# Performance work log

Hardware: AMD Instinct MI355X
Metric: run time of the kernel (lower is better)

The kernel has to match this reference:

```python
import jax, jax.numpy as jnp
import numpy as np

DIM, NCOND, K, NFLOWS, HID = 8, 16, 5, 2, 8
TB = 3.0                      # tail bound B
CMAX = NCOND + DIM - 1        # 23, max conditioning width (zero-padded)
MINW = MINH = MIND = 1e-3


def _fcnn(x, W1, b1, W2, b2, W3, b3):
    h = jnp.tanh(x @ W1.T + b1)
    h = jnp.tanh(h @ W2.T + b2)
    return h @ W3.T + b3


def _rqs_fwd(x, uw, uh, ud, tb):
    # x: [N]; uw, uh: [N, K] (already softmaxed+scaled by caller, re-softmaxed
    # here to match the original RQS implementation); ud: [N, K+1] (padded)
    nb = uw.shape[-1]
    widths = MINW + (1.0 - MINW * nb) * jax.nn.softmax(uw, axis=-1)
    cumw = jnp.pad(jnp.cumsum(widths, axis=-1), ((0, 0), (1, 0)))
    cumw = (2.0 * tb) * cumw - tb
    cumw = cumw.at[:, 0].set(-tb).at[:, -1].set(tb)
    widths = cumw[:, 1:] - cumw[:, :-1]
    heights = MINH + (1.0 - MINH * nb) * jax.nn.softmax(uh, axis=-1)
    cumh = jnp.pad(jnp.cumsum(heights, axis=-1), ((0, 0), (1, 0)))
    cumh = (2.0 * tb) * cumh - tb
    cumh = cumh.at[:, 0].set(-tb).at[:, -1].set(tb)
    heights = cumh[:, 1:] - cumh[:, :-1]
    derivs = MIND + jax.nn.softplus(ud)
    # searchsorted with eps on last edge
    idx = (jnp.sum(x[:, None] >= cumw.at[:, -1].add(1e-6), axis=-1) - 1)[:, None]
    take = lambda a: jnp.take_along_axis(a, idx, axis=-1)[:, 0]
    icw, ibw, ich, ih = take(cumw), take(widths), take(cumh), take(heights)
    idelta = take(heights / widths)
    d0, d1 = take(derivs), take(derivs[:, 1:])
    th = (x - icw) / ibw
    t2, tomt = th * th, th * (1.0 - th)
    den = idelta + (d0 + d1 - 2.0 * idelta) * tomt
    z = ich + ih * (idelta * t2 + d0 * tomt) / den
    ld = jnp.log(idelta ** 2 * (d1 * t2 + 2.0 * idelta * tomt + d0 * (1.0 - th) ** 2)) - 2.0 * jnp.log(den)
    return z, ld


def _unconstrained_rqs(x, W, H, D, tb):
    inside = (x >= -tb) & (x <= tb)
    const = float(np.log(np.exp(1.0 - MIND) - 1.0))
    Dp = jnp.pad(D, ((0, 0), (1, 1)), constant_values=const)
    z_in, ld_in = _rqs_fwd(jnp.clip(x, -tb, tb), W, H, Dp, tb)
    return jnp.where(inside, z_in, x), jnp.where(inside, ld_in, 0.0)


def setup_inputs() -> dict:
    key = jax.random.key(0)
    ks = jax.random.split(key, 16)
    N = 524288
    s = 0.3
    inp = {
        "x_inp": jax.random.normal(ks[0], (N, DIM), jnp.float32),
        "cond_inp": jax.random.normal(ks[1], (N, NCOND), jnp.float32),
        # init (base-dist) nets, one per dim; first layer zero-padded to CMAX
        "Wi1": s * jax.random.normal(ks[2], (DIM, HID, CMAX), jnp.float32),
        "bi1": s * jax.random.normal(ks[3], (DIM, HID), jnp.float32),
        "Wi2": s * jax.random.normal(ks[4], (DIM, HID, HID), jnp.float32),
        "bi2": s * jax.random.normal(ks[5], (DIM, HID), jnp.float32),
        "Wi3": s * jax.random.normal(ks[6], (DIM, 2, HID), jnp.float32),
        "bi3": s * jax.random.normal(ks[7], (DIM, 2), jnp.float32),
        # flow nets, per (dim, flow)
        "Wf1": s * jax.random.normal(ks[8], (DIM, NFLOWS, HID, CMAX), jnp.float32),
        "bf1": s * jax.random.normal(ks[9], (DIM, NFLOWS, HID), jnp.float32),
        "Wf2": s * jax.random.normal(ks[10], (DIM, NFLOWS, HID, HID), jnp.float32),
        "bf2": s * jax.random.normal(ks[11], (DIM, NFLOWS, HID), jnp.float32),
        "Wf3": s * jax.random.normal(ks[12], (DIM, NFLOWS, 3 * K - 1, HID), jnp.float32),
        "bf3": s * jax.random.normal(ks[13], (DIM, NFLOWS, 3 * K - 1), jnp.float32),
    }
    return inp


def reference(x_inp, cond_inp, Wi1, bi1, Wi2, bi2, Wi3, bi3,
              Wf1, bf1, Wf2, bf2, Wf3, bf3):
    N = x_inp.shape[0]
    logp_cols = []
    for jd in range(DIM):
        pad = jnp.zeros((N, CMAX - NCOND - jd), x_inp.dtype)
        cond_jd = jnp.concatenate([cond_inp, x_inp[:, :jd], pad], axis=1)  # [N, CMAX]
        # gumbel base-dist params
        outg = _fcnn(cond_jd, Wi1[jd], bi1[jd], Wi2[jd], bi2[jd], Wi3[jd], bi3[jd])
        mu, sig = outg[:, 0], jnp.exp(outg[:, 1])
        x = x_inp[:, jd]
        ld_sum = jnp.zeros((N,), x_inp.dtype)
        for jf in range(NFLOWS):
            out = _fcnn(cond_jd, Wf1[jd, jf], bf1[jd, jf], Wf2[jd, jf], bf2[jd, jf],
                        Wf3[jd, jf], bf3[jd, jf])  # [N, 3K-1]
            W = 2.0 * TB * jax.nn.softmax(out[:, :K], axis=1)
            H = 2.0 * TB * jax.nn.softmax(out[:, K:2 * K], axis=1)
            D = jax.nn.softplus(out[:, 2 * K:])
            x, ld = _unconstrained_rqs(x, W, H, D, TB)
            ld_sum = ld_sum + ld
        z = (x - mu) / sig
        lp = -(z + jnp.exp(-z)) - jnp.log(sig)  # Gumbel log_prob
        lp = jnp.where(jnp.isnan(lp) | jnp.isinf(lp), -100.0, lp)
        logp_cols.append(ld_sum + lp)
    return jnp.sum(jnp.stack(logp_cols, axis=1), axis=1)
```

## Files before the change

### kernel.cpp

```cpp
#include <hip/hip_runtime.h>
#include <math.h>

__device__ __forceinline__ float rcp_(float x) { return __fdividef(1.0f, x); }

__device__ __forceinline__ float tanh_(float x) {
    float t = x * x;
    float p = t + 378.0f;
    p = fmaf(p, t, 17325.0f);
    p = fmaf(p, t, 135135.0f);
    float q = fmaf(28.0f, t, 3150.0f);
    q = fmaf(q, t, 62370.0f);
    q = fmaf(q, t, 135135.0f);
    float r = (x * p) * rcp_(q);
    return fminf(fmaxf(r, -1.0f), 1.0f);
}

__device__ __forceinline__ float sp2_(float x) {
    return __logf(2.0f + __expf(x));
}

__device__ __forceinline__ void dsm5_(float o0, float o1, float o2, float o3, float o4,
                                      float* __restrict__ w) {
    float e0 = __expf(o0), e1 = __expf(o1), e2 = __expf(o2),
          e3 = __expf(o3), e4 = __expf(o4);
    float inv = 6.0f * rcp_(((e0 + e1) + (e2 + e3)) + e4);
    float f0 = __expf(e0 * inv);
    float f1 = __expf(e1 * inv);
    float f2 = __expf(e2 * inv);
    float f3 = __expf(e3 * inv);
    float f4 = __expf(e4 * inv);
    float t = 0.995f * rcp_(((f0 + f1) + (f2 + f3)) + f4);
    w[0] = fmaf(f0, t, 0.001f);
    w[1] = fmaf(f1, t, 0.001f);
    w[2] = fmaf(f2, t, 0.001f);
    w[3] = fmaf(f3, t, 0.001f);
    w[4] = fmaf(f4, t, 0.001f);
}

__global__ __launch_bounds__(512, 4)
void nsf_kernel(const float* __restrict__ x_inp, const float* __restrict__ cond_inp,
                const float* __restrict__ Wi1, const float* __restrict__ bi1,
                const float* __restrict__ Wi2, const float* __restrict__ bi2,
                const float* __restrict__ Wi3, const float* __restrict__ bi3,
                const float* __restrict__ Wf1, const float* __restrict__ bf1,
                const float* __restrict__ Wf2, const float* __restrict__ bf2,
                const float* __restrict__ Wf3, const float* __restrict__ bf3,
                float* __restrict__ out, int N)
{
    const int lane = threadIdx.x;
    const int jd   = threadIdx.y;
    const int jdu  = __builtin_amdgcn_readfirstlane(jd);
    int s = blockIdx.x * 64 + lane;
    int sl = (s < N) ? s : (N - 1);

    float cond[23];
    float xcur;
    {
        const float4* cp = (const float4*)(cond_inp + (size_t)sl * 16);
        float4 c0 = cp[0], c1 = cp[1], c2 = cp[2], c3 = cp[3];
        cond[0]=c0.x;  cond[1]=c0.y;  cond[2]=c0.z;  cond[3]=c0.w;
        cond[4]=c1.x;  cond[5]=c1.y;  cond[6]=c1.z;  cond[7]=c1.w;
        cond[8]=c2.x;  cond[9]=c2.y;  cond[10]=c2.z; cond[11]=c2.w;
        cond[12]=c3.x; cond[13]=c3.y; cond[14]=c3.z; cond[15]=c3.w;

        const float4* xp = (const float4*)(x_inp + (size_t)sl * 8);
        float4 a = xp[0], b = xp[1];
        float xv[8] = {a.x, a.y, a.z, a.w, b.x, b.y, b.z, b.w};
#pragma unroll
        for (int t = 0; t < 7; ++t)
            cond[16 + t] = (t < jd) ? xv[t] : 0.0f;
        xcur = xv[jd];
    }

    float g0, g1;
    {
        const float* W1 = Wi1 + (size_t)jdu * 184;
        const float* b1 = bi1 + jdu * 8;
        const float* W2 = Wi2 + (size_t)jdu * 64;
        const float* b2 = bi2 + jdu * 8;
        const float* W3 = Wi3 + (size_t)jdu * 16;
        const float* b3 = bi3 + jdu * 2;
        float h1[8], h2[8];
#pragma unroll
        for (int i = 0; i < 8; ++i) {
            float a = b1[i];
#pragma unroll
            for (int c = 0; c < 23; ++c) a = fmaf(W1[i * 23 + c], cond[c], a);
            h1[i] = tanh_(a);
        }
#pragma unroll
        for (int i = 0; i < 8; ++i) {
            float a = b2[i];
#pragma unroll
            for (int c = 0; c < 8; ++c) a = fmaf(W2[i * 8 + c], h1[c], a);
            h2[i] = tanh_(a);
        }
        g0 = b3[0]; g1 = b3[1];
#pragma unroll
        for (int c = 0; c < 8; ++c) {
            g0 = fmaf(W3[c], h2[c], g0);
            g1 = fmaf(W3[8 + c], h2[c], g1);
        }
    }

    float ldsum = 0.0f;
#pragma unroll
    for (int jf = 0; jf < 2; ++jf) {
        const int nf = jdu * 2 + jf;
        const float* F1  = Wf1 + (size_t)nf * 184;
        const float* fb1 = bf1 + nf * 8;
        const float* F2  = Wf2 + (size_t)nf * 64;
        const float* fb2 = bf2 + nf * 8;
        const float* F3  = Wf3 + (size_t)nf * 112;
        const float* fb3 = bf3 + nf * 14;

        float h1[8], h2[8];
#pragma unroll
        for (int i = 0; i < 8; ++i) {
            float a = fb1[i];
#pragma unroll
            for (int c = 0; c < 23; ++c) a = fmaf(F1[i * 23 + c], cond[c], a);
            h1[i] = tanh_(a);
        }
#pragma unroll
        for (int i = 0; i < 8; ++i) {
            float a = fb2[i];
#pragma unroll
            for (int c = 0; c < 8; ++c) a = fmaf(F2[i * 8 + c], h1[c], a);
            h2[i] = tanh_(a);
        }
        float o[14];
#pragma unroll
        for (int i = 0; i < 14; ++i) {
            float a = fb3[i];
#pragma unroll
            for (int c = 0; c < 8; ++c) a = fmaf(F3[i * 8 + c], h2[c], a);
            o[i] = a;
        }

        float wv[5], hv[5];
        dsm5_(o[0], o[1], o[2], o[3], o[4], wv);
        dsm5_(o[5], o[6], o[7], o[8], o[9], hv);
        float di1 = sp2_(o[10]) + 0.001f;
        float di2 = sp2_(o[11]) + 0.001f;
        float di3 = sp2_(o[12]) + 0.001f;
        float di4 = sp2_(o[13]) + 0.001f;

        float xc = fminf(fmaxf(xcur, -3.0f), 3.0f);

        float runw = wv[0], runh = hv[0];
        float cwL = -3.0f, chL = -3.0f;
        float cwR = fmaf(6.0f, runw, -3.0f);
        float chR = fmaf(6.0f, runh, -3.0f);
        float icw = cwL, ibw = cwR - cwL, ich = chL, ihh = chR - chL;
        float d0 = 1.0f, d1 = di1;
#pragma unroll
        for (int k = 1; k < 5; ++k) {
            cwL = cwR; chL = chR;
            runw += wv[k]; runh += hv[k];
            cwR = (k == 4) ? 3.0f : fmaf(6.0f, runw, -3.0f);
            chR = (k == 4) ? 3.0f : fmaf(6.0f, runh, -3.0f);
            float dk0 = (k == 1) ? di1 : (k == 2) ? di2 : (k == 3) ? di3 : di4;
            float dk1 = (k == 1) ? di2 : (k == 2) ? di3 : (k == 3) ? di4 : 1.0f;
            bool sel = (xc >= cwL);
            icw = sel ? cwL : icw;
            ibw = sel ? (cwR - cwL) : ibw;
            ich = sel ? chL : ich;
            ihh = sel ? (chR - chL) : ihh;
            d0  = sel ? dk0 : d0;
            d1  = sel ? dk1 : d1;
        }

        float rb     = rcp_(ibw);
        float idelta = ihh * rb;
        float th     = (xc - icw) * rb;
        float t2     = th * th;
        float omt    = 1.0f - th;
        float tomt   = th * omt;
        float den    = fmaf(fmaf(-2.0f, idelta, d0 + d1), tomt, idelta);
        float rden   = rcp_(den);
        float xn     = fmaf(ihh * fmaf(idelta, t2, d0 * tomt), rden, ich);
        float num    = (idelta * idelta) *
                       fmaf(d1, t2, fmaf(idelta + idelta, tomt, d0 * (omt * omt)));
        float ldi    = __logf((num * rden) * rden);

        bool inside = (xcur >= -3.0f) && (xcur <= 3.0f);
        xcur  = inside ? xn : xcur;
        ldsum = inside ? (ldsum + ldi) : ldsum;
    }

    float z  = (xcur - g0) * __expf(-g1);
    float ez = __expf(-z);
    float lp = -(z + ez) - g1;
    if (isnan(lp) || isinf(lp)) lp = -100.0f;
    float col = ldsum + lp;

    __shared__ float red[8][64];
    red[jd][lane] = col;
    __syncthreads();
    if (jd == 0 && s < N) {
        float acc = red[0][lane];
#pragma unroll
        for (int j = 1; j < 8; ++j) acc += red[j][lane];
        out[s] = acc;
    }
}

extern "C" void kernel_launch(void* const* d_in, const int* in_sizes, int n_in,
                              void* d_out, int out_size, void* d_ws, size_t ws_size,
                              hipStream_t stream) {
    const float* x_inp    = (const float*)d_in[0];
    const float* cond_inp = (const float*)d_in[1];
    const float* Wi1 = (const float*)d_in[2];
    const float* bi1 = (const float*)d_in[3];
    const float* Wi2 = (const float*)d_in[4];
    const float* bi2 = (const float*)d_in[5];
    const float* Wi3 = (const float*)d_in[6];
    const float* bi3 = (const float*)d_in[7];
    const float* Wf1 = (const float*)d_in[8];
    const float* bf1 = (const float*)d_in[9];
    const float* Wf2 = (const float*)d_in[10];
    const float* bf2 = (const float*)d_in[11];
    const float* Wf3 = (const float*)d_in[12];
    const float* bf3 = (const float*)d_in[13];
    float* out = (float*)d_out;

    int N = out_size;
    int grid = (N + 63) / 64;
    dim3 block(64, 8, 1);
    hipLaunchKernelGGL(nsf_kernel, dim3(grid), block, 0, stream,
                       x_inp, cond_inp, Wi1, bi1, Wi2, bi2, Wi3, bi3,
                       Wf1, bf1, Wf2, bf2, Wf3, bf3, out, N);
}
```

Measured before the change: 236.0 us.

## Map flow dimension to grid y and accumulate columns with atomics

Each block now handles 512 samples for a single flow dimension taken from blockIdx.y, replacing the 64x8 block layout that summed the eight dimensions through shared memory. A separate kernel first zeroes the output, and each thread then atomically adds its column's log-prob into it. This removes the shared-memory reduction and __syncthreads, and dimension-indexed weight loads stay uniform across the block. In exchange it costs an extra launch, 8x atomic traffic to the output, and a nondeterministic summation order. The zero kernel covers only N/4 float4s, so it assumes N is a multiple of 4.

```diff
diff --git a/kernel.cpp b/kernel.cpp
--- a/kernel.cpp
+++ b/kernel.cpp
@@ -37,7 +37,13 @@
     w[4] = fmaf(f4, t, 0.001f);
 }
 
-__global__ __launch_bounds__(512, 4)
+__global__ __launch_bounds__(512)
+void zero_out(float* __restrict__ out, int n4) {
+    int i = blockIdx.x * blockDim.x + threadIdx.x;
+    if (i < n4) ((float4*)out)[i] = (float4){0.0f, 0.0f, 0.0f, 0.0f};
+}
+
+__global__ __launch_bounds__(512)
 void nsf_kernel(const float* __restrict__ x_inp, const float* __restrict__ cond_inp,
                 const float* __restrict__ Wi1, const float* __restrict__ bi1,
                 const float* __restrict__ Wi2, const float* __restrict__ bi2,
@@ -47,10 +53,8 @@
                 const float* __restrict__ Wf3, const float* __restrict__ bf3,
                 float* __restrict__ out, int N)
 {
-    const int lane = threadIdx.x;
-    const int jd   = threadIdx.y;
-    const int jdu  = __builtin_amdgcn_readfirstlane(jd);
-    int s = blockIdx.x * 64 + lane;
+    const int jd = blockIdx.y;
+    int s = blockIdx.x * 512 + threadIdx.x;
     int sl = (s < N) ? s : (N - 1);
 
     float cond[23];
@@ -69,17 +73,19 @@
 #pragma unroll
         for (int t = 0; t < 7; ++t)
             cond[16 + t] = (t < jd) ? xv[t] : 0.0f;
-        xcur = xv[jd];
+        xcur = xv[0];
+#pragma unroll
+        for (int t = 1; t < 8; ++t) xcur = (jd == t) ? xv[t] : xcur;
     }
 
     float g0, g1;
     {
-        const float* W1 = Wi1 + (size_t)jdu * 184;
-        const float* b1 = bi1 + jdu * 8;
-        const float* W2 = Wi2 + (size_t)jdu * 64;
-        const float* b2 = bi2 + jdu * 8;
-        const float* W3 = Wi3 + (size_t)jdu * 16;
-        const float* b3 = bi3 + jdu * 2;
+        const float* W1 = Wi1 + (size_t)jd * 184;
+        const float* b1 = bi1 + jd * 8;
+        const float* W2 = Wi2 + (size_t)jd * 64;
+        const float* b2 = bi2 + jd * 8;
+        const float* W3 = Wi3 + (size_t)jd * 16;
+        const float* b3 = bi3 + jd * 2;
         float h1[8], h2[8];
 #pragma unroll
         for (int i = 0; i < 8; ++i) {
@@ -106,7 +112,7 @@
     float ldsum = 0.0f;
 #pragma unroll
     for (int jf = 0; jf < 2; ++jf) {
-        const int nf = jdu * 2 + jf;
+        const int nf = jd * 2 + jf;
         const float* F1  = Wf1 + (size_t)nf * 184;
         const float* fb1 = bf1 + nf * 8;
         const float* F2  = Wf2 + (size_t)nf * 64;
@@ -193,17 +199,8 @@
     float ez = __expf(-z);
     float lp = -(z + ez) - g1;
     if (isnan(lp) || isinf(lp)) lp = -100.0f;
-    float col = ldsum + lp;
-
-    __shared__ float red[8][64];
-    red[jd][lane] = col;
-    __syncthreads();
-    if (jd == 0 && s < N) {
-        float acc = red[0][lane];
-#pragma unroll
-        for (int j = 1; j < 8; ++j) acc += red[j][lane];
-        out[s] = acc;
-    }
+
+    if (s < N) atomicAdd(&out[s], ldsum + lp);
 }
 
 extern "C" void kernel_launch(void* const* d_in, const int* in_sizes, int n_in,
@@ -226,9 +223,11 @@
     float* out = (float*)d_out;
 
     int N = out_size;
-    int grid = (N + 63) / 64;
-    dim3 block(64, 8, 1);
-    hipLaunchKernelGGL(nsf_kernel, dim3(grid), block, 0, stream,
+    int n4 = N / 4;
+    hipLaunchKernelGGL(zero_out, dim3((n4 + 511) / 512), dim3(512), 0, stream, out, n4);
+
+    dim3 grid((N + 511) / 512, 8, 1);
+    hipLaunchKernelGGL(nsf_kernel, grid, dim3(512), 0, stream,
                        x_inp, cond_inp, Wi1, bi1, Wi2, bi2, Wi3, bi3,
                        Wf1, bf1, Wf2, bf2, Wf3, bf3, out, N);
 }
```

Result: slower. 268.2 us (+13.6%).

## Split the two flow MLPs across a second thread dimension with shared-memory handoff

Applied to the files above, without the earlier changes.

Doubles the block to 64x8x2 so that each z-slice computes one of the two flow-conditioner MLPs in parallel. Slice 0 writes its 14 outputs to shared memory and then computes the Gumbel base MLP, while slice 1 evaluates both spline transforms in sequence. The aim is to expose more thread-level parallelism and cut per-thread serial work. In exchange it adds about 36KB of LDS, extra barriers and a load imbalance between the slices, and the 1024-thread blocks with relaxed launch bounds may reduce occupancy.

```diff
diff --git a/kernel.cpp b/kernel.cpp
--- a/kernel.cpp
+++ b/kernel.cpp
@@ -37,7 +37,7 @@
     w[4] = fmaf(f4, t, 0.001f);
 }
 
-__global__ __launch_bounds__(512, 4)
+__global__ __launch_bounds__(1024)
 void nsf_kernel(const float* __restrict__ x_inp, const float* __restrict__ cond_inp,
                 const float* __restrict__ Wi1, const float* __restrict__ bi1,
                 const float* __restrict__ Wi2, const float* __restrict__ bi2,
@@ -49,9 +49,15 @@
 {
     const int lane = threadIdx.x;
     const int jd   = threadIdx.y;
+    const int nz   = threadIdx.z;
     const int jdu  = __builtin_amdgcn_readfirstlane(jd);
+    const int nzu  = __builtin_amdgcn_readfirstlane(nz);
     int s = blockIdx.x * 64 + lane;
     int sl = (s < N) ? s : (N - 1);
+
+    __shared__ float o0s[8][64][14];
+    __shared__ float gs[8][64][2];
+    __shared__ float red[8][64];
 
     float cond[23];
     float xcur;
@@ -69,11 +75,52 @@
 #pragma unroll
         for (int t = 0; t < 7; ++t)
             cond[16 + t] = (t < jd) ? xv[t] : 0.0f;
-        xcur = xv[jd];
-    }
-
-    float g0, g1;
+        xcur = xv[0];
+#pragma unroll
+        for (int t = 1; t < 8; ++t) xcur = (jd == t) ? xv[t] : xcur;
+    }
+
+    float o[14];
     {
+        const int nf = 2 * jdu + nzu;
+        const float* F1  = Wf1 + (size_t)nf * 184;
+        const float* fb1 = bf1 + nf * 8;
+        const float* F2  = Wf2 + (size_t)nf * 64;
+        const float* fb2 = bf2 + nf * 8;
+        const float* F3  = Wf3 + (size_t)nf * 112;
+        const float* fb3 = bf3 + nf * 14;
+
+        float h1[8], h2[8];
+#pragma unroll
+        for (int i = 0; i < 8; ++i) {
+            float a = fb1[i];
+#pragma unroll
+            for (int c = 0; c < 23; ++c) a = fmaf(F1[i * 23 + c], cond[c], a);
+            h1[i] = tanh_(a);
+        }
+#pragma unroll
+        for (int i = 0; i < 8; ++i) {
+            float a = fb2[i];
+#pragma unroll
+            for (int c = 0; c < 8; ++c) a = fmaf(F2[i * 8 + c], h1[c], a);
+            h2[i] = tanh_(a);
+        }
+#pragma unroll
+        for (int i = 0; i < 14; ++i) {
+            float a = fb3[i];
+#pragma unroll
+            for (int c = 0; c < 8; ++c) a = fmaf(F3[i * 8 + c], h2[c], a);
+            o[i] = a;
+        }
+    }
+    if (nz == 0) {
+#pragma unroll
+        for (int i = 0; i < 14; ++i) o0s[jd][lane][i] = o[i];
+    }
+    __syncthreads();
+
+    float col = 0.0f;
+    if (nz == 0) {
         const float* W1 = Wi1 + (size_t)jdu * 184;
         const float* b1 = bi1 + jdu * 8;
         const float* W2 = Wi2 + (size_t)jdu * 64;
@@ -95,110 +142,88 @@
             for (int c = 0; c < 8; ++c) a = fmaf(W2[i * 8 + c], h1[c], a);
             h2[i] = tanh_(a);
         }
-        g0 = b3[0]; g1 = b3[1];
+        float g0 = b3[0], g1 = b3[1];
 #pragma unroll
         for (int c = 0; c < 8; ++c) {
             g0 = fmaf(W3[c], h2[c], g0);
             g1 = fmaf(W3[8 + c], h2[c], g1);
         }
-    }
-
-    float ldsum = 0.0f;
-#pragma unroll
-    for (int jf = 0; jf < 2; ++jf) {
-        const int nf = jdu * 2 + jf;
-        const float* F1  = Wf1 + (size_t)nf * 184;
-        const float* fb1 = bf1 + nf * 8;
-        const float* F2  = Wf2 + (size_t)nf * 64;
-        const float* fb2 = bf2 + nf * 8;
-        const float* F3  = Wf3 + (size_t)nf * 112;
-        const float* fb3 = bf3 + nf * 14;
-
-        float h1[8], h2[8];
-#pragma unroll
-        for (int i = 0; i < 8; ++i) {
-            float a = fb1[i];
-#pragma unroll
-            for (int c = 0; c < 23; ++c) a = fmaf(F1[i * 23 + c], cond[c], a);
-            h1[i] = tanh_(a);
-        }
-#pragma unroll
-        for (int i = 0; i < 8; ++i) {
-            float a = fb2[i];
-#pragma unroll
-            for (int c = 0; c < 8; ++c) a = fmaf(F2[i * 8 + c], h1[c], a);
-            h2[i] = tanh_(a);
-        }
-        float o[14];
-#pragma unroll
-        for (int i = 0; i < 14; ++i) {
-            float a = fb3[i];
-#pragma unroll
-            for (int c = 0; c < 8; ++c) a = fmaf(F3[i * 8 + c], h2[c], a);
-            o[i] = a;
-        }
-
-        float wv[5], hv[5];
-        dsm5_(o[0], o[1], o[2], o[3], o[4], wv);
-        dsm5_(o[5], o[6], o[7], o[8], o[9], hv);
-        float di1 = sp2_(o[10]) + 0.001f;
-        float di2 = sp2_(o[11]) + 0.001f;
-        float di3 = sp2_(o[12]) + 0.001f;
-        float di4 = sp2_(o[13]) + 0.001f;
-
-        float xc = fminf(fmaxf(xcur, -3.0f), 3.0f);
-
-        float runw = wv[0], runh = hv[0];
-        float cwL = -3.0f, chL = -3.0f;
-        float cwR = fmaf(6.0f, runw, -3.0f);
-        float chR = fmaf(6.0f, runh, -3.0f);
-        float icw = cwL, ibw = cwR - cwL, ich = chL, ihh = chR - chL;
-        float d0 = 1.0f, d1 = di1;
-#pragma unroll
-        for (int k = 1; k < 5; ++k) {
-            cwL = cwR; chL = chR;
-            runw += wv[k]; runh += hv[k];
-            cwR = (k == 4) ? 3.0f : fmaf(6.0f, runw, -3.0f);
-            chR = (k == 4) ? 3.0f : fmaf(6.0f, runh, -3.0f);
-            float dk0 = (k == 1) ? di1 : (k == 2) ? di2 : (k == 3) ? di3 : di4;
-            float dk1 = (k == 1) ? di2 : (k == 2) ? di3 : (k == 3) ? di4 : 1.0f;
-            bool sel = (xc >= cwL);
-            icw = sel ? cwL : icw;
-            ibw = sel ? (cwR - cwL) : ibw;
-            ich = sel ? chL : ich;
-            ihh = sel ? (chR - chL) : ihh;
-            d0  = sel ? dk0 : d0;
-            d1  = sel ? dk1 : d1;
-        }
-
-        float rb     = rcp_(ibw);
-        float idelta = ihh * rb;
-        float th     = (xc - icw) * rb;
-        float t2     = th * th;
-        float omt    = 1.0f - th;
-        float tomt   = th * omt;
-        float den    = fmaf(fmaf(-2.0f, idelta, d0 + d1), tomt, idelta);
-        float rden   = rcp_(den);
-        float xn     = fmaf(ihh * fmaf(idelta, t2, d0 * tomt), rden, ich);
-        float num    = (idelta * idelta) *
-                       fmaf(d1, t2, fmaf(idelta + idelta, tomt, d0 * (omt * omt)));
-        float ldi    = __logf((num * rden) * rden);
-
-        bool inside = (xcur >= -3.0f) && (xcur <= 3.0f);
-        xcur  = inside ? xn : xcur;
-        ldsum = inside ? (ldsum + ldi) : ldsum;
-    }
-
-    float z  = (xcur - g0) * __expf(-g1);
-    float ez = __expf(-z);
-    float lp = -(z + ez) - g1;
-    if (isnan(lp) || isinf(lp)) lp = -100.0f;
-    float col = ldsum + lp;
-
-    __shared__ float red[8][64];
-    red[jd][lane] = col;
+        gs[jd][lane][0] = g0;
+        gs[jd][lane][1] = g1;
+    } else {
+        float ldsum = 0.0f;
+        auto spline = [&](const float* __restrict__ oo) {
+            float wv[5], hv[5];
+            dsm5_(oo[0], oo[1], oo[2], oo[3], oo[4], wv);
+            dsm5_(oo[5], oo[6], oo[7], oo[8], oo[9], hv);
+            float di1 = sp2_(oo[10]) + 0.001f;
+            float di2 = sp2_(oo[11]) + 0.001f;
+            float di3 = sp2_(oo[12]) + 0.001f;
+            float di4 = sp2_(oo[13]) + 0.001f;
+
+            float xc = fminf(fmaxf(xcur, -3.0f), 3.0f);
+
+            float runw = wv[0], runh = hv[0];
+            float cwL = -3.0f, chL = -3.0f;
+            float cwR = fmaf(6.0f, runw, -3.0f);
+            float chR = fmaf(6.0f, runh, -3.0f);
+            float icw = cwL, ibw = cwR - cwL, ich = chL, ihh = chR - chL;
+            float d0 = 1.0f, d1 = di1;
+#pragma unroll
+            for (int k = 1; k < 5; ++k) {
+                cwL = cwR; chL = chR;
+                runw += wv[k]; runh += hv[k];
+                cwR = (k == 4) ? 3.0f : fmaf(6.0f, runw, -3.0f);
+                chR = (k == 4) ? 3.0f : fmaf(6.0f, runh, -3.0f);
+                float dk0 = (k == 1) ? di1 : (k == 2) ? di2 : (k == 3) ? di3 : di4;
+                float dk1 = (k == 1) ? di2 : (k == 2) ? di3 : (k == 3) ? di4 : 1.0f;
+                bool sel = (xc >= cwL);
+                icw = sel ? cwL : icw;
+                ibw = sel ? (cwR - cwL) : ibw;
+                ich = sel ? chL : ich;
+                ihh = sel ? (chR - chL) : ihh;
+                d0  = sel ? dk0 : d0;
+                d1  = sel ? dk1 : d1;
+            }
+
+            float rb     = rcp_(ibw);
+            float idelta = ihh * rb;
+            float th     = (xc - icw) * rb;
+            float t2     = th * th;
+            float omt    = 1.0f - th;
+            float tomt   = th * omt;
+            float den    = fmaf(fmaf(-2.0f, idelta, d0 + d1), tomt, idelta);
+            float rden   = rcp_(den);
+            float xn     = fmaf(ihh * fmaf(idelta, t2, d0 * tomt), rden, ich);
+            float num    = (idelta * idelta) *
+                           fmaf(d1, t2, fmaf(idelta + idelta, tomt, d0 * (omt * omt)));
+            float ldi    = __logf((num * rden) * rden);
+
+            bool inside = (xcur >= -3.0f) && (xcur <= 3.0f);
+            xcur  = inside ? xn : xcur;
+            ldsum = inside ? (ldsum + ldi) : ldsum;
+        };
+        float oo[14];
+#pragma unroll
+        for (int i = 0; i < 14; ++i) oo[i] = o0s[jd][lane][i];
+        spline(oo);
+        spline(o);
+        col = ldsum;
+    }
     __syncthreads();
-    if (jd == 0 && s < N) {
+
+    if (nz == 1) {
+        float g0 = gs[jd][lane][0];
+        float g1 = gs[jd][lane][1];
+        float z  = (xcur - g0) * __expf(-g1);
+        float ez = __expf(-z);
+        float lp = -(z + ez) - g1;
+        if (isnan(lp) || isinf(lp)) lp = -100.0f;
+        red[jd][lane] = col + lp;
+    }
+    __syncthreads();
+
+    if (nz == 1 && jd == 0 && s < N) {
         float acc = red[0][lane];
 #pragma unroll
         for (int j = 1; j < 8; ++j) acc += red[j][lane];
@@ -227,7 +252,7 @@
 
     int N = out_size;
     int grid = (N + 63) / 64;
-    dim3 block(64, 8, 1);
+    dim3 block(64, 8, 2);
     hipLaunchKernelGGL(nsf_kernel, dim3(grid), block, 0, stream,
                        x_inp, cond_inp, Wi1, bi1, Wi2, bi2, Wi3, bi3,
                        Wf1, bf1, Wf2, bf2, Wf3, bf3, out, N);
```

Result: slower. 248.6 us (+5.3%).
